# Performance work log

Measured on AMD Instinct MI355X. Metric: run time of the kernel, lower is better.

Reference implementation:

```python
import jax, jax.numpy as jnp
import numpy as np

K_SIZE = 5

def setup_inputs() -> dict:
    key = jax.random.key(0)
    images = jax.random.normal(key, (8, 128, 128, 32), dtype=jnp.float32)
    return {"images": images}

def reference(images) -> jnp.ndarray:
    # images: [B, H, W, C] with H == W (module assumes square images)
    k = K_SIZE
    B, H, W, C = images.shape
    p = (k - 1) // 2
    # ZeroPadding2D((p, p))
    padded = jnp.pad(images, ((0, 0), (p, p), (p, p), (0, 0)))
    # wh_indices: row/col start offsets; element (ki, kj) of patch at (i, j)
    # reads padded[i + ki, j + kj] (a1 = row repeated over kj, a2 = tiled cols).
    ri = jnp.arange(H)[:, None] + jnp.arange(k)  # [H, k]
    ci = jnp.arange(W)[:, None] + jnp.arange(k)  # [W, k]
    # Advanced indexing -> [B, H, W, k, k, C]
    patches = padded[:, ri[:, None, :, None], ci[None, :, None, :], :]
    # reshape to [B, H, W, k*k*C] (ki, kj, c ordering, matching tf.gather_nd)
    return patches.reshape(B, H, W, k * k * C)
```

## Files before the change

### kernel.cpp

```cpp
#include <hip/hip_runtime.h>


constexpr int KK   = 5;
constexpr int PAD  = 2;
constexpr int CH4  = 8;
constexpr int HH   = 128, WW = 128, BB = 8;
constexpr int ROW_F4     = WW * CH4;
constexpr int OUT_ROW_F4 = WW * KK * KK * CH4;
constexpr int THREADS    = 512;
constexpr int STAGE_F4   = KK * ROW_F4;
constexpr int NWG        = BB * HH;
constexpr int STORES_PER_THREAD = OUT_ROW_F4 / THREADS;

typedef float f32x4 __attribute__((ext_vector_type(4)));

__global__ void __launch_bounds__(THREADS) extract_patch_kernel(
        const f32x4* __restrict__ in, f32x4* __restrict__ out) {
    __shared__ f32x4 lds[STAGE_F4];

    int bid = blockIdx.x;
    int lin = (bid & 7) * (NWG / 8) + (bid >> 3);
    int b = lin >> 7;
    int h = lin & (HH - 1);

    int tid = threadIdx.x;

    #pragma unroll
    for (int i = 0; i < STAGE_F4 / THREADS; ++i) {
        int j  = tid + i * THREADS;
        int r5 = j >> 10;
        int gr = h + r5 - PAD;
        bool ok = (unsigned)gr < (unsigned)HH;
        int grc = ok ? gr : 0;
        f32x4 v = in[(size_t)(b * HH + grc) * ROW_F4 + (j & (ROW_F4 - 1))];
        f32x4 z = 0.f;
        lds[j] = ok ? v : z;
    }
    __syncthreads();

    f32x4* rowout = out + (size_t)lin * OUT_ROW_F4;
    #pragma unroll 5
    for (int it = 0; it < STORES_PER_THREAD; ++it) {
        int j  = tid + it * THREADS;
        int w  = j / 200;
        int r  = j - w * 200;
        int kq = r >> 3;
        int c4 = r & 7;
        int kh = (kq * 205) >> 10;
        int kw = kq - kh * 5;
        int pc = w + kw - PAD;
        bool ok = (unsigned)pc < (unsigned)WW;
        f32x4 v = lds[kh * ROW_F4 + (pc & (WW - 1)) * CH4 + c4];
        f32x4 z = 0.f;
        v = ok ? v : z;
        __builtin_nontemporal_store(v, &rowout[j]);
    }
}

extern "C" void kernel_launch(void* const* d_in, const int* in_sizes, int n_in,
                              void* d_out, int out_size, void* d_ws, size_t ws_size,
                              hipStream_t stream) {
    const f32x4* images = (const f32x4*)d_in[0];
    f32x4* out = (f32x4*)d_out;
    extract_patch_kernel<<<NWG, THREADS, 0, stream>>>(images, out);
}
```

Before: 81.98 us.

## Process four output rows per block with a rolling LDS ring buffer

```diff
diff --git a/kernel.cpp b/kernel.cpp
--- a/kernel.cpp
+++ b/kernel.cpp
@@ -7,53 +7,74 @@
 constexpr int HH   = 128, WW = 128, BB = 8;
 constexpr int ROW_F4     = WW * CH4;
 constexpr int OUT_ROW_F4 = WW * KK * KK * CH4;
-constexpr int THREADS    = 512;
-constexpr int STAGE_F4   = KK * ROW_F4;
-constexpr int NWG        = BB * HH;
-constexpr int STORES_PER_THREAD = OUT_ROW_F4 / THREADS;
+constexpr int THREADS    = 1024;
+constexpr int ROWS_PER_BLK = 4;
+constexpr int NWG        = BB * HH / ROWS_PER_BLK;
+constexpr int SLOTS      = 8;
 
 typedef float f32x4 __attribute__((ext_vector_type(4)));
 
 __global__ void __launch_bounds__(THREADS) extract_patch_kernel(
         const f32x4* __restrict__ in, f32x4* __restrict__ out) {
-    __shared__ f32x4 lds[STAGE_F4];
+    __shared__ f32x4 lds[SLOTS * ROW_F4];
 
     int bid = blockIdx.x;
     int lin = (bid & 7) * (NWG / 8) + (bid >> 3);
-    int b = lin >> 7;
-    int h = lin & (HH - 1);
+    int b     = lin >> 5;
+    int h0    = (lin & 31) * ROWS_PER_BLK;
 
     int tid = threadIdx.x;
+    const f32x4* img = in + (size_t)b * HH * ROW_F4;
 
-    #pragma unroll
-    for (int i = 0; i < STAGE_F4 / THREADS; ++i) {
-        int j  = tid + i * THREADS;
-        int r5 = j >> 10;
-        int gr = h + r5 - PAD;
-        bool ok = (unsigned)gr < (unsigned)HH;
-        int grc = ok ? gr : 0;
-        f32x4 v = in[(size_t)(b * HH + grc) * ROW_F4 + (j & (ROW_F4 - 1))];
-        f32x4 z = 0.f;
-        lds[j] = ok ? v : z;
+    {
+        f32x4 v0[5];
+        #pragma unroll
+        for (int i = 0; i < 5; ++i) {
+            int gr = h0 - PAD + i;
+            v0[i] = 0.f;
+            if ((unsigned)gr < (unsigned)HH)
+                v0[i] = img[(size_t)gr * ROW_F4 + tid];
+        }
+        #pragma unroll
+        for (int i = 0; i < 5; ++i) {
+            int gr = h0 - PAD + i;
+            lds[(gr & (SLOTS - 1)) * ROW_F4 + tid] = v0[i];
+        }
     }
     __syncthreads();
 
-    f32x4* rowout = out + (size_t)lin * OUT_ROW_F4;
-    #pragma unroll 5
-    for (int it = 0; it < STORES_PER_THREAD; ++it) {
-        int j  = tid + it * THREADS;
-        int w  = j / 200;
-        int r  = j - w * 200;
-        int kq = r >> 3;
-        int c4 = r & 7;
-        int kh = (kq * 205) >> 10;
-        int kw = kq - kh * 5;
-        int pc = w + kw - PAD;
-        bool ok = (unsigned)pc < (unsigned)WW;
-        f32x4 v = lds[kh * ROW_F4 + (pc & (WW - 1)) * CH4 + c4];
-        f32x4 z = 0.f;
-        v = ok ? v : z;
-        __builtin_nontemporal_store(v, &rowout[j]);
+    for (int r = 0; r < ROWS_PER_BLK; ++r) {
+        int h = h0 + r;
+
+        bool do_pf = (r < ROWS_PER_BLK - 1);
+        int  gr_pf = h + 3;
+        f32x4 pf = 0.f;
+        if (do_pf && (unsigned)gr_pf < (unsigned)HH)
+            pf = img[(size_t)gr_pf * ROW_F4 + tid];
+
+        f32x4* rowout = out + ((size_t)lin * ROWS_PER_BLK + r) * OUT_ROW_F4;
+        #pragma unroll 5
+        for (int it = 0; it < OUT_ROW_F4 / THREADS; ++it) {
+            int j  = tid + it * THREADS;
+            int w  = j / 200;
+            int rr = j - w * 200;
+            int kq = rr >> 3;
+            int c4 = rr & 7;
+            int kh = (kq * 205) >> 10;
+            int kw = kq - kh * 5;
+            int pc = w + kw - PAD;
+            int gr = h + kh - PAD;
+            int slot = gr & (SLOTS - 1);
+            bool ok = (unsigned)pc < (unsigned)WW;
+            f32x4 v = lds[slot * ROW_F4 + (pc & (WW - 1)) * CH4 + c4];
+            f32x4 z = 0.f;
+            v = ok ? v : z;
+            __builtin_nontemporal_store(v, &rowout[j]);
+        }
+
+        if (do_pf)
+            lds[(gr_pf & (SLOTS - 1)) * ROW_F4 + tid] = pf;
+        __syncthreads();
     }
 }
 
```

Result: faster. 79.78 us (-2.7%).

## Read input directly from global memory instead of staging rows in LDS

Applied to the files above, without the earlier changes.

```diff
diff --git a/kernel.cpp b/kernel.cpp
--- a/kernel.cpp
+++ b/kernel.cpp
@@ -1,56 +1,42 @@
 #include <hip/hip_runtime.h>
 
 
-constexpr int KK   = 5;
 constexpr int PAD  = 2;
 constexpr int CH4  = 8;
 constexpr int HH   = 128, WW = 128, BB = 8;
 constexpr int ROW_F4     = WW * CH4;
-constexpr int OUT_ROW_F4 = WW * KK * KK * CH4;
-constexpr int THREADS    = 512;
-constexpr int STAGE_F4   = KK * ROW_F4;
+constexpr int OUT_ROW_F4 = WW * 25 * CH4;
+constexpr int THREADS    = 1024;
 constexpr int NWG        = BB * HH;
-constexpr int STORES_PER_THREAD = OUT_ROW_F4 / THREADS;
 
 typedef float f32x4 __attribute__((ext_vector_type(4)));
 
 __global__ void __launch_bounds__(THREADS) extract_patch_kernel(
         const f32x4* __restrict__ in, f32x4* __restrict__ out) {
-    __shared__ f32x4 lds[STAGE_F4];
-
     int bid = blockIdx.x;
     int lin = (bid & 7) * (NWG / 8) + (bid >> 3);
     int b = lin >> 7;
     int h = lin & (HH - 1);
 
     int tid = threadIdx.x;
+    const f32x4* img = in + (size_t)b * HH * ROW_F4;
+    f32x4* rowout = out + (size_t)lin * OUT_ROW_F4;
 
-    #pragma unroll
-    for (int i = 0; i < STAGE_F4 / THREADS; ++i) {
-        int j  = tid + i * THREADS;
-        int r5 = j >> 10;
-        int gr = h + r5 - PAD;
-        bool ok = (unsigned)gr < (unsigned)HH;
-        int grc = ok ? gr : 0;
-        f32x4 v = in[(size_t)(b * HH + grc) * ROW_F4 + (j & (ROW_F4 - 1))];
-        f32x4 z = 0.f;
-        lds[j] = ok ? v : z;
-    }
-    __syncthreads();
-
-    f32x4* rowout = out + (size_t)lin * OUT_ROW_F4;
     #pragma unroll 5
-    for (int it = 0; it < STORES_PER_THREAD; ++it) {
+    for (int it = 0; it < OUT_ROW_F4 / THREADS; ++it) {
         int j  = tid + it * THREADS;
         int w  = j / 200;
-        int r  = j - w * 200;
-        int kq = r >> 3;
-        int c4 = r & 7;
+        int rr = j - w * 200;
+        int kq = rr >> 3;
+        int c4 = rr & 7;
         int kh = (kq * 205) >> 10;
         int kw = kq - kh * 5;
         int pc = w + kw - PAD;
-        bool ok = (unsigned)pc < (unsigned)WW;
-        f32x4 v = lds[kh * ROW_F4 + (pc & (WW - 1)) * CH4 + c4];
+        int gr = h + kh - PAD;
+        bool ok = ((unsigned)pc < (unsigned)WW) &
+                  ((unsigned)gr < (unsigned)HH);
+        f32x4 v = img[(size_t)(gr & (HH - 1)) * ROW_F4
+                      + (pc & (WW - 1)) * CH4 + c4];
         f32x4 z = 0.f;
         v = ok ? v : z;
         __builtin_nontemporal_store(v, &rowout[j]);
```

Measured after the change: 75.81 us (median of 2 runs). -7.5%, faster.
